# Kernel optimization log

Hardware: AMD Instinct MI355X
Metric: run time of the kernel (lower is better)

The kernel has to match this reference:

```python
import jax, jax.numpy as jnp
import numpy as np
import math

N, T, D, H = 2, 4096, 768, 12
DH = D // H


def setup_inputs() -> dict:
    key = jax.random.key(0)
    ks = jax.random.split(key, 6)
    x = jax.random.normal(ks[0], (N, T, D), dtype=jnp.float32)
    # key-padding mask: True = masked out; mask the last quarter of positions
    mask = jnp.broadcast_to(jnp.arange(T) >= (3 * T) // 4, (N, T))
    scale = 0.02
    Wq = jax.random.normal(ks[1], (D, D), dtype=jnp.float32) * scale
    Wk = jax.random.normal(ks[2], (D, D), dtype=jnp.float32) * scale
    Wv = jax.random.normal(ks[3], (D, D), dtype=jnp.float32) * scale
    Wo = jax.random.normal(ks[4], (D, D), dtype=jnp.float32) * scale
    zb = jnp.zeros((D,), dtype=jnp.float32)
    return {"x": x, "mask": mask, "Wq": Wq, "bq": zb, "Wk": Wk, "bk": zb,
            "Wv": Wv, "bv": zb, "Wo": Wo, "bo": zb}


def reference(x, mask, Wq, bq, Wk, bk, Wv, bv, Wo, bo):
    n, t, d = x.shape
    h, dh = H, d // H
    # torch Linear: y = x @ W.T + b
    def proj(W, b):
        return (x @ W.T + b).reshape(n, t, h, dh).transpose(0, 2, 1, 3)  # [n,h,t,dh]
    q = proj(Wq, bq)
    k = proj(Wk, bk)
    v = proj(Wv, bv)
    s = jnp.einsum('nhqd,nhkd->nhqk', q, k) / math.sqrt(dh)  # [n,h,t,t]
    s = jnp.where(mask[:, None, None, :], -jnp.inf, s)
    p = jax.nn.softmax(s, axis=-1)
    # dropout prob 0.0 / eval mode -> identity
    a = jnp.einsum('nhqk,nhkd->nhqd', p, v)  # [n,h,t,dh]
    a = a.transpose(0, 2, 1, 3).reshape(n, t, d)
    return a @ Wo.T + bo
```

## Files before the change

kernel.cpp:

```cpp
#include <hip/hip_runtime.h>
#include <hip/hip_bf16.h>
#include <stdint.h>

#define T_SEQ 4096
#define DM    768
#define NHEAD 12
#define DHEAD 64
#define NBAT  2
#define LOG2E 1.4426950408889634f

typedef __bf16 bf16x8 __attribute__((ext_vector_type(8)));
typedef float  f32x4  __attribute__((ext_vector_type(4)));

static __device__ __forceinline__ unsigned short f2bf(float f) {
  unsigned int u = __builtin_bit_cast(unsigned int, f);
  u += 0x7FFFu + ((u >> 16) & 1u);
  return (unsigned short)(u >> 16);
}
static __device__ __forceinline__ unsigned short f2bf_hw(float f) {
  __hip_bfloat16 h = __float2bfloat16(f);
  return __builtin_bit_cast(unsigned short, h);
}
static __device__ __forceinline__ unsigned int pk2(float lo, float hi) {
  return (unsigned int)f2bf_hw(lo) | ((unsigned int)f2bf_hw(hi) << 16);
}
static __device__ __forceinline__ void gll16(const void* g, void* l) {
  __builtin_amdgcn_global_load_lds(
      (const __attribute__((address_space(1))) unsigned int*)g,
      (__attribute__((address_space(3))) unsigned int*)l, 16, 0, 0);
}
static __device__ __forceinline__ bf16x8 ldfrag(const unsigned short* p) {
  const unsigned short* q = (const unsigned short*)__builtin_assume_aligned(p, 16);
  bf16x8 v;
  __builtin_memcpy(&v, q, 16);
  return v;
}
static __device__ __forceinline__ void st8(unsigned short* p, uint2 v) {
  __builtin_memcpy(__builtin_assume_aligned(p, 8), &v, 8);
}
static __device__ __forceinline__ uint2 ld8(const unsigned short* p) {
  uint2 v;
  __builtin_memcpy(&v, __builtin_assume_aligned(p, 8), 8);
  return v;
}

__global__ void cvt_kernel(const float* __restrict__ s, unsigned short* __restrict__ d, int n) {
  int i = (blockIdx.x * 256 + threadIdx.x) * 4;
  if (i < n) {
    float4 v = *(const float4*)(s + i);
    ushort4 o;
    o.x = f2bf(v.x); o.y = f2bf(v.y); o.z = f2bf(v.z); o.w = f2bf(v.w);
    *(ushort4*)(d + i) = o;
  }
}
__global__ void cvt4_kernel(const float* __restrict__ s0, const float* __restrict__ s1,
                            const float* __restrict__ s2, const float* __restrict__ s3,
                            unsigned short* __restrict__ d0, unsigned short* __restrict__ d1,
                            unsigned short* __restrict__ d2, unsigned short* __restrict__ d3,
                            int n) {
  int w = blockIdx.y;
  const float* sp = (w == 0) ? s0 : (w == 1) ? s1 : (w == 2) ? s2 : s3;
  unsigned short* dp = (w == 0) ? d0 : (w == 1) ? d1 : (w == 2) ? d2 : d3;
  int i = (blockIdx.x * 256 + threadIdx.x) * 4;
  if (i < n) {
    float4 v = *(const float4*)(sp + i);
    ushort4 o;
    o.x = f2bf(v.x); o.y = f2bf(v.y); o.z = f2bf(v.z); o.w = f2bf(v.w);
    *(ushort4*)(dp + i) = o;
  }
}

__global__ void init_kernel(int* __restrict__ kmx) {
  if (threadIdx.x < NBAT) { kmx[threadIdx.x] = 0; kmx[NBAT + threadIdx.x] = T_SEQ; }
}

__global__ void build_bias_kernel(const unsigned char* __restrict__ mraw,
                                  float* __restrict__ bias,
                                  int* __restrict__ kmx) {
  int idx = blockIdx.x * 256 + threadIdx.x;
  int is_u8 = (mraw[(3 * T_SEQ) / 4] != 0);
  int masked;
  if (is_u8) masked = (mraw[idx] != 0);
  else       masked = (((const int*)mraw)[idx] != 0);
  bias[idx] = masked ? -1e9f : 0.0f;
  __shared__ int smax, smin;
  if (threadIdx.x == 0) { smax = 0; smin = T_SEQ; }
  __syncthreads();
  int pos = idx & (T_SEQ - 1);
  if (!masked) atomicMax(&smax, pos + 1);
  else         atomicMin(&smin, pos);
  __syncthreads();
  if (threadIdx.x == 0) {
    atomicMax(&kmx[idx >> 12], smax);
    atomicMin(&kmx[NBAT + (idx >> 12)], smin);
  }
}

template <int MODE>
__global__ __launch_bounds__(256, 2) void gemm128(
    const unsigned short* __restrict__ A,
    const unsigned short* __restrict__ W0, const unsigned short* __restrict__ W1,
    const unsigned short* __restrict__ W2,
    const float* __restrict__ Bb0, const float* __restrict__ Bb1,
    const float* __restrict__ Bb2,
    void* __restrict__ O0, void* __restrict__ O1, void* __restrict__ O2) {
  constexpr int NT = (MODE == 0) ? 8 : 4;
  constexpr int NROWS = NT * 32;
  __shared__ __align__(16) unsigned short lA[128 * 64];
  __shared__ __align__(16) unsigned short lB[NROWS * 64];
  const int t = threadIdx.x;
  const int lane = t & 63, quad = lane >> 4, l16 = lane & 15;
  const int wave = t >> 6;
  const int moff = (wave & 1) * 64, noff = (wave >> 1) * (NT * 16);
  const int m0 = blockIdx.x * 128;
  const int by = blockIdx.y;
  const unsigned short* W;
  const float* Bb;
  int o0, wsel = 0;
  if constexpr (MODE == 0) {
    wsel = by / 3;
    o0 = (by % 3) * 256;
    W  = (wsel == 0) ? W0  : ((wsel == 1) ? W1  : W2);
    Bb = (wsel == 0) ? Bb0 : ((wsel == 1) ? Bb1 : Bb2);
  } else {
    o0 = by * 128; W = W0; Bb = Bb0;
  }
  f32x4 acc[4][NT];
#pragma unroll
  for (int i = 0; i < 4; ++i)
#pragma unroll
    for (int j = 0; j < NT; ++j) acc[i][j] = (f32x4){0.f, 0.f, 0.f, 0.f};

  for (int k0 = 0; k0 < DM; k0 += 64) {
#pragma unroll
    for (int i = 0; i < 4; ++i) {
      int c = i * 256 + t;
      int r = c >> 3;
      int qc = (c & 7) ^ (r & 7);
      gll16(A + (size_t)(m0 + r) * DM + k0 + qc * 8, &lA[(i * 256 + (t & 192)) * 8]);
    }
#pragma unroll
    for (int i = 0; i < NT; ++i) {
      int c = i * 256 + t;
      int r = c >> 3;
      int qc = (c & 7) ^ (r & 7);
      gll16(W + (size_t)(o0 + r) * DM + k0 + qc * 8, &lB[(i * 256 + (t & 192)) * 8]);
    }
    __syncthreads();
    bf16x8 af[4][2];
#pragma unroll
    for (int mt = 0; mt < 4; ++mt) {
      int r = moff + mt * 16 + l16;
#pragma unroll
      for (int s = 0; s < 2; ++s)
        af[mt][s] = ldfrag(&lA[(r * 8 + ((s * 4 + quad) ^ (r & 7))) * 8]);
    }
#pragma unroll
    for (int nt = 0; nt < NT; ++nt) {
      int r = noff + nt * 16 + l16;
      bf16x8 b0 = ldfrag(&lB[(r * 8 + ((quad) ^ (r & 7))) * 8]);
      bf16x8 b1 = ldfrag(&lB[(r * 8 + ((4 + quad) ^ (r & 7))) * 8]);
#pragma unroll
      for (int mt = 0; mt < 4; ++mt) {
        acc[mt][nt] = __builtin_amdgcn_mfma_f32_16x16x32_bf16(af[mt][0], b0, acc[mt][nt], 0, 0, 0);
        acc[mt][nt] = __builtin_amdgcn_mfma_f32_16x16x32_bf16(af[mt][1], b1, acc[mt][nt], 0, 0, 0);
      }
    }
    __syncthreads();
  }
#pragma unroll
  for (int nt = 0; nt < NT; ++nt) {
    int o = o0 + noff + nt * 16 + l16;
    float bias = Bb[o];
    if (MODE == 0 && wsel == 2) {
      int h = o >> 6, d = o & 63;
#pragma unroll
      for (int mt = 0; mt < 4; ++mt) {
        int m = m0 + moff + mt * 16 + quad * 4;
        int n = m >> 12, tb = m & (T_SEQ - 1);
        uint2 w;
        w.x = pk2(acc[mt][nt][0] + bias, acc[mt][nt][1] + bias);
        w.y = pk2(acc[mt][nt][2] + bias, acc[mt][nt][3] + bias);
        *(uint2*)((unsigned short*)O2 +
                  ((size_t)(n * NHEAD + h) * DHEAD + d) * T_SEQ + tb) = w;
      }
      continue;
    }
#pragma unroll
    for (int mt = 0; mt < 4; ++mt) {
#pragma unroll
      for (int r = 0; r < 4; ++r) {
        int m = m0 + moff + mt * 16 + quad * 4 + r;
        float v = acc[mt][nt][r] + bias;
        if constexpr (MODE == 0) {
          int n = m >> 12, tt = m & (T_SEQ - 1);
          int h = o >> 6, d = o & 63;
          if (wsel == 0)
            ((unsigned short*)O0)[((size_t)(n * NHEAD + h) * T_SEQ + tt) * DHEAD + d] = f2bf(v * (0.125f * LOG2E));
          else
            ((unsigned short*)O1)[((size_t)(n * NHEAD + h) * T_SEQ + tt) * DHEAD + d] = f2bf(v);
        } else {
          ((float*)O0)[(size_t)m * DM + o] = v;
        }
      }
    }
  }
}

__global__ __launch_bounds__(256, 3) void flash_kernel(
    const unsigned short* __restrict__ Q, const unsigned short* __restrict__ K,
    const unsigned short* __restrict__ VT, const float* __restrict__ bias,
    const int* __restrict__ kmx, unsigned short* __restrict__ Aout) {
  __shared__ __align__(16) unsigned short lK[128 * 64];
  __shared__ __align__(16) unsigned short lV[64 * 128];
  const int t = threadIdx.x;
  const int lane = t & 63, quad = lane >> 4, l16 = lane & 15;
  const int wave = t >> 6;
  const int nh = blockIdx.y;
  const int n = nh / NHEAD, h = nh % NHEAD;
  const int q0 = blockIdx.x * 128;
  const size_t base = (size_t)nh * T_SEQ * DHEAD;

  bf16x8 qf[2][2];
#pragma unroll
  for (int qt = 0; qt < 2; ++qt) {
    int qrow = q0 + wave * 32 + qt * 16 + l16;
    qf[qt][0] = ldfrag(Q + base + (size_t)qrow * DHEAD + quad * 8);
    qf[qt][1] = ldfrag(Q + base + (size_t)qrow * DHEAD + 32 + quad * 8);
  }

  bf16x8 vone;
#pragma unroll
  for (int i = 0; i < 8; ++i) vone[i] = (__bf16)1.0f;

  f32x4 oacc[2][4], oaccl[2];
#pragma unroll
  for (int qt = 0; qt < 2; ++qt) {
#pragma unroll
    for (int dt = 0; dt < 4; ++dt) oacc[qt][dt] = (f32x4){0.f, 0.f, 0.f, 0.f};
    oaccl[qt] = (f32x4){0.f, 0.f, 0.f, 0.f};
  }

  const int km = kmx[n], fm = kmx[NBAT + n];
  int ntiles = (km + 127) >> 7;
  if (ntiles > (T_SEQ >> 7)) ntiles = T_SEQ >> 7;
  const float* brow = bias + (size_t)n * T_SEQ;

  const int idxA = ((((quad & 1) << 1) * 16) + l16) << 2;
  const int idxB = idxA + 64;
  const bool hiq = (quad >= 2);

  for (int it = 0; it < ntiles; ++it) {
    const int j0 = it << 7;
#pragma unroll
    for (int i = 0; i < 4; ++i) {
      int c = i * 256 + t;
      int r = c >> 3;
      int qc = (c & 7) ^ (r & 7);
      gll16(K + base + (size_t)(j0 + r) * DHEAD + qc * 8, &lK[(i * 256 + (t & 192)) * 8]);
    }
#pragma unroll
    for (int i = 0; i < 4; ++i) {
      int c = i * 256 + t;
      int r = c >> 4;
      int qc = (c & 15) ^ (r & 15);
      gll16(VT + base + (size_t)r * T_SEQ + j0 + qc * 8, &lV[(i * 256 + (t & 192)) * 8]);
    }
    __syncthreads();

    f32x4 sacc[2][8];
#pragma unroll
    for (int qt = 0; qt < 2; ++qt)
#pragma unroll
      for (int nt = 0; nt < 8; ++nt) sacc[qt][nt] = (f32x4){0.f, 0.f, 0.f, 0.f};
#pragma unroll
    for (int nt = 0; nt < 8; ++nt) {
      int r = nt * 16 + l16;
      bf16x8 k0f = ldfrag(&lK[(r * 8 + (quad ^ (r & 7))) * 8]);
      bf16x8 k1f = ldfrag(&lK[(r * 8 + ((4 + quad) ^ (r & 7))) * 8]);
#pragma unroll
      for (int qt = 0; qt < 2; ++qt) {
        sacc[qt][nt] = __builtin_amdgcn_mfma_f32_16x16x32_bf16(k0f, qf[qt][0], sacc[qt][nt], 0, 0, 0);
        sacc[qt][nt] = __builtin_amdgcn_mfma_f32_16x16x32_bf16(k1f, qf[qt][1], sacc[qt][nt], 0, 0, 0);
      }
    }
    if (j0 + 128 > fm) {
#pragma unroll
      for (int nt = 0; nt < 8; ++nt) {
        float4 bv = *(const float4*)&brow[j0 + nt * 16 + quad * 4];
#pragma unroll
        for (int qt = 0; qt < 2; ++qt) {
          sacc[qt][nt][0] += bv.x; sacc[qt][nt][1] += bv.y;
          sacc[qt][nt][2] += bv.z; sacc[qt][nt][3] += bv.w;
        }
      }
    }
    unsigned int pd[2][8][2];
#pragma unroll
    for (int qt = 0; qt < 2; ++qt)
#pragma unroll
      for (int nt = 0; nt < 8; ++nt) {
        pd[qt][nt][0] = pk2(__builtin_exp2f(sacc[qt][nt][0]), __builtin_exp2f(sacc[qt][nt][1]));
        pd[qt][nt][1] = pk2(__builtin_exp2f(sacc[qt][nt][2]), __builtin_exp2f(sacc[qt][nt][3]));
      }
#pragma unroll
    for (int kb = 0; kb < 4; ++kb) {
      bf16x8 pb[2];
#pragma unroll
      for (int qt = 0; qt < 2; ++qt) {
        unsigned int t0, t1;
        uint4 bw;
        t0 = (unsigned int)__builtin_amdgcn_ds_bpermute(idxA, (int)pd[qt][2 * kb][0]);
        t1 = (unsigned int)__builtin_amdgcn_ds_bpermute(idxA, (int)pd[qt][2 * kb + 1][0]);
        bw.x = hiq ? t1 : t0;
        t0 = (unsigned int)__builtin_amdgcn_ds_bpermute(idxA, (int)pd[qt][2 * kb][1]);
        t1 = (unsigned int)__builtin_amdgcn_ds_bpermute(idxA, (int)pd[qt][2 * kb + 1][1]);
        bw.y = hiq ? t1 : t0;
        t0 = (unsigned int)__builtin_amdgcn_ds_bpermute(idxB, (int)pd[qt][2 * kb][0]);
        t1 = (unsigned int)__builtin_amdgcn_ds_bpermute(idxB, (int)pd[qt][2 * kb + 1][0]);
        bw.z = hiq ? t1 : t0;
        t0 = (unsigned int)__builtin_amdgcn_ds_bpermute(idxB, (int)pd[qt][2 * kb][1]);
        t1 = (unsigned int)__builtin_amdgcn_ds_bpermute(idxB, (int)pd[qt][2 * kb + 1][1]);
        bw.w = hiq ? t1 : t0;
        pb[qt] = __builtin_bit_cast(bf16x8, bw);
      }
#pragma unroll
      for (int dt = 0; dt < 4; ++dt) {
        int rv = dt * 16 + l16;
        bf16x8 vf = ldfrag(&lV[(rv * 16 + ((kb * 4 + quad) ^ (rv & 15))) * 8]);
#pragma unroll
        for (int qt = 0; qt < 2; ++qt)
          oacc[qt][dt] = __builtin_amdgcn_mfma_f32_16x16x32_bf16(vf, pb[qt], oacc[qt][dt], 0, 0, 0);
      }
#pragma unroll
      for (int qt = 0; qt < 2; ++qt)
        oaccl[qt] = __builtin_amdgcn_mfma_f32_16x16x32_bf16(vone, pb[qt], oaccl[qt], 0, 0, 0);
    }
    __syncthreads();
  }
  unsigned short* lO = &lK[wave * (32 * 68)];
#pragma unroll
  for (int qt = 0; qt < 2; ++qt) {
    float l = oaccl[qt][0];
    float rl = (l > 0.f) ? 1.0f / l : 0.f;
#pragma unroll
    for (int dt = 0; dt < 4; ++dt) {
      uint2 w;
      w.x = pk2(oacc[qt][dt][0] * rl, oacc[qt][dt][1] * rl);
      w.y = pk2(oacc[qt][dt][2] * rl, oacc[qt][dt][3] * rl);
      st8(lO + (qt * 16 + l16) * 68 + dt * 16 + quad * 4, w);
    }
  }
#pragma unroll
  for (int it2 = 0; it2 < 8; ++it2) {
    int rowq = it2 * 4 + quad;
    uint2 w = ld8(lO + rowq * 68 + l16 * 4);
    int tt = q0 + wave * 32 + rowq;
    *(uint2*)(Aout + (size_t)(n * T_SEQ + tt) * DM + h * DHEAD + l16 * 4) = w;
  }
}

extern "C" void kernel_launch(void* const* d_in, const int* in_sizes, int n_in,
                              void* d_out, int out_size, void* d_ws, size_t ws_size,
                              hipStream_t stream) {
  const float*         x  = (const float*)d_in[0];
  const unsigned char* mk = (const unsigned char*)d_in[1];
  const float* Wq = (const float*)d_in[2];
  const float* bq = (const float*)d_in[3];
  const float* Wk = (const float*)d_in[4];
  const float* bk = (const float*)d_in[5];
  const float* Wv = (const float*)d_in[6];
  const float* bv = (const float*)d_in[7];
  const float* Wo = (const float*)d_in[8];
  const float* bo = (const float*)d_in[9];

  const int xe = NBAT * T_SEQ * DM;
  const int we = DM * DM;
  const size_t xb_bytes = (size_t)xe * 2;
  const size_t wb_bytes = (size_t)we * 2;
  const size_t kv_bytes = (size_t)NBAT * NHEAD * T_SEQ * DHEAD * 2;

  auto rnd = [](size_t b) { return (b + 255) & ~(size_t)255; };
  size_t need = rnd(xb_bytes) + 4 * rnd(wb_bytes) + 2 * rnd(kv_bytes) +
                rnd((size_t)NBAT * T_SEQ * 4) + 256;
  if (ws_size < need) return;

  char* ws = (char*)d_ws;
  size_t off = 0;
  auto alloc = [&](size_t b) { char* p = ws + off; off += rnd(b); return p; };
  unsigned short* x_b  = (unsigned short*)alloc(xb_bytes);
  unsigned short* wq_b = (unsigned short*)alloc(wb_bytes);
  unsigned short* wk_b = (unsigned short*)alloc(wb_bytes);
  unsigned short* wv_b = (unsigned short*)alloc(wb_bytes);
  unsigned short* wo_b = (unsigned short*)alloc(wb_bytes);
  unsigned short* k_ws  = (unsigned short*)alloc(kv_bytes);
  unsigned short* vt_ws = (unsigned short*)alloc(kv_bytes);
  float* bias = (float*)alloc((size_t)NBAT * T_SEQ * 4);
  int* kmx    = (int*)alloc(256);
  unsigned short* q_ws = (unsigned short*)d_out;
  unsigned short* a_ws = x_b;

  init_kernel<<<1, 64, 0, stream>>>(kmx);
  cvt_kernel<<<xe / 1024, 256, 0, stream>>>(x, x_b, xe);
  cvt4_kernel<<<dim3(we / 1024, 4), 256, 0, stream>>>(
      Wq, Wk, Wv, Wo, wq_b, wk_b, wv_b, wo_b, we);
  build_bias_kernel<<<(NBAT * T_SEQ) / 256, 256, 0, stream>>>(mk, bias, kmx);
  gemm128<0><<<dim3((NBAT * T_SEQ) / 128, 9), 256, 0, stream>>>(
      x_b, wq_b, wk_b, wv_b, bq, bk, bv, q_ws, k_ws, vt_ws);
  flash_kernel<<<dim3(T_SEQ / 128, NBAT * NHEAD), 256, 0, stream>>>(
      q_ws, k_ws, vt_ws, bias, kmx, a_ws);
  gemm128<1><<<dim3((NBAT * T_SEQ) / 128, DM / 128), 256, 0, stream>>>(
      a_ws, wo_b, wo_b, wo_b, bo, bo, bo, d_out, d_out, d_out);
  (void)in_sizes; (void)n_in; (void)out_size;
}
```

Before: 316.1 us.

## Use single-wave flash blocks reading K/V directly and retile projection GEMMs

The flash kernel becomes one wave per block covering 32 query rows. It drops the LDS staging of K and V and the block barriers, loading MFMA fragments straight from global memory. Block indices are remapped so that neighbouring blocks share heads, which is meant to help L2 reuse of K/V. Separately, both GEMMs get narrower N tiles (192 and 96 columns) with more blocks in the grid, and the QKV GEMM's occupancy bound is raised to 3. The risk is that many more uncoalesced global loads of K/V replace shared-memory reuse across four waves.

```diff
diff --git a/kernel.cpp b/kernel.cpp
--- a/kernel.cpp
+++ b/kernel.cpp
@@ -97,14 +97,14 @@
 }
 
 template <int MODE>
-__global__ __launch_bounds__(256, 2) void gemm128(
+__global__ __launch_bounds__(256, (MODE == 0) ? 3 : 2) void gemm128(
     const unsigned short* __restrict__ A,
     const unsigned short* __restrict__ W0, const unsigned short* __restrict__ W1,
     const unsigned short* __restrict__ W2,
     const float* __restrict__ Bb0, const float* __restrict__ Bb1,
     const float* __restrict__ Bb2,
     void* __restrict__ O0, void* __restrict__ O1, void* __restrict__ O2) {
-  constexpr int NT = (MODE == 0) ? 8 : 4;
+  constexpr int NT = (MODE == 0) ? 6 : 3;
   constexpr int NROWS = NT * 32;
   __shared__ __align__(16) unsigned short lA[128 * 64];
   __shared__ __align__(16) unsigned short lB[NROWS * 64];
@@ -118,12 +118,12 @@
   const float* Bb;
   int o0, wsel = 0;
   if constexpr (MODE == 0) {
-    wsel = by / 3;
-    o0 = (by % 3) * 256;
+    wsel = by >> 2;
+    o0 = (by & 3) * 192;
     W  = (wsel == 0) ? W0  : ((wsel == 1) ? W1  : W2);
     Bb = (wsel == 0) ? Bb0 : ((wsel == 1) ? Bb1 : Bb2);
   } else {
-    o0 = by * 128; W = W0; Bb = Bb0;
+    o0 = by * 96; W = W0; Bb = Bb0;
   }
   f32x4 acc[4][NT];
 #pragma unroll
@@ -207,24 +207,26 @@
   }
 }
 
-__global__ __launch_bounds__(256, 3) void flash_kernel(
+__global__ __launch_bounds__(64, 3) void flash_kernel(
     const unsigned short* __restrict__ Q, const unsigned short* __restrict__ K,
     const unsigned short* __restrict__ VT, const float* __restrict__ bias,
     const int* __restrict__ kmx, unsigned short* __restrict__ Aout) {
-  __shared__ __align__(16) unsigned short lK[128 * 64];
-  __shared__ __align__(16) unsigned short lV[64 * 128];
-  const int t = threadIdx.x;
-  const int lane = t & 63, quad = lane >> 4, l16 = lane & 15;
-  const int wave = t >> 6;
-  const int nh = blockIdx.y;
-  const int n = nh / NHEAD, h = nh % NHEAD;
-  const int q0 = blockIdx.x * 128;
+  __shared__ __align__(16) unsigned short lO[32 * 68];
+  const int lane = threadIdx.x;
+  const int quad = lane >> 4, l16 = lane & 15;
+  const int b = blockIdx.x;
+  const int slot = b >> 3;
+  const int nh = (b & 7) * 3 + (slot % 3);
+  const int q0 = (slot / 3) * 32;
+  const int n = nh / NHEAD, h = nh - n * NHEAD;
   const size_t base = (size_t)nh * T_SEQ * DHEAD;
+  const unsigned short* Kb = K + base + (size_t)l16 * DHEAD + quad * 8;
+  const unsigned short* Vb = VT + base + (size_t)l16 * T_SEQ + quad * 8;
 
   bf16x8 qf[2][2];
 #pragma unroll
   for (int qt = 0; qt < 2; ++qt) {
-    int qrow = q0 + wave * 32 + qt * 16 + l16;
+    int qrow = q0 + qt * 16 + l16;
     qf[qt][0] = ldfrag(Q + base + (size_t)qrow * DHEAD + quad * 8);
     qf[qt][1] = ldfrag(Q + base + (size_t)qrow * DHEAD + 32 + quad * 8);
   }
@@ -252,22 +254,6 @@
 
   for (int it = 0; it < ntiles; ++it) {
     const int j0 = it << 7;
-#pragma unroll
-    for (int i = 0; i < 4; ++i) {
-      int c = i * 256 + t;
-      int r = c >> 3;
-      int qc = (c & 7) ^ (r & 7);
-      gll16(K + base + (size_t)(j0 + r) * DHEAD + qc * 8, &lK[(i * 256 + (t & 192)) * 8]);
-    }
-#pragma unroll
-    for (int i = 0; i < 4; ++i) {
-      int c = i * 256 + t;
-      int r = c >> 4;
-      int qc = (c & 15) ^ (r & 15);
-      gll16(VT + base + (size_t)r * T_SEQ + j0 + qc * 8, &lV[(i * 256 + (t & 192)) * 8]);
-    }
-    __syncthreads();
-
     f32x4 sacc[2][8];
 #pragma unroll
     for (int qt = 0; qt < 2; ++qt)
@@ -275,9 +261,9 @@
       for (int nt = 0; nt < 8; ++nt) sacc[qt][nt] = (f32x4){0.f, 0.f, 0.f, 0.f};
 #pragma unroll
     for (int nt = 0; nt < 8; ++nt) {
-      int r = nt * 16 + l16;
-      bf16x8 k0f = ldfrag(&lK[(r * 8 + (quad ^ (r & 7))) * 8]);
-      bf16x8 k1f = ldfrag(&lK[(r * 8 + ((4 + quad) ^ (r & 7))) * 8]);
+      const unsigned short* kr = Kb + (size_t)(j0 + nt * 16) * DHEAD;
+      bf16x8 k0f = ldfrag(kr);
+      bf16x8 k1f = ldfrag(kr + 32);
 #pragma unroll
       for (int qt = 0; qt < 2; ++qt) {
         sacc[qt][nt] = __builtin_amdgcn_mfma_f32_16x16x32_bf16(k0f, qf[qt][0], sacc[qt][nt], 0, 0, 0);
@@ -326,8 +312,7 @@
       }
 #pragma unroll
       for (int dt = 0; dt < 4; ++dt) {
-        int rv = dt * 16 + l16;
-        bf16x8 vf = ldfrag(&lV[(rv * 16 + ((kb * 4 + quad) ^ (rv & 15))) * 8]);
+        bf16x8 vf = ldfrag(Vb + (size_t)(dt * 16) * T_SEQ + j0 + kb * 32);
 #pragma unroll
         for (int qt = 0; qt < 2; ++qt)
           oacc[qt][dt] = __builtin_amdgcn_mfma_f32_16x16x32_bf16(vf, pb[qt], oacc[qt][dt], 0, 0, 0);
@@ -336,9 +321,7 @@
       for (int qt = 0; qt < 2; ++qt)
         oaccl[qt] = __builtin_amdgcn_mfma_f32_16x16x32_bf16(vone, pb[qt], oaccl[qt], 0, 0, 0);
     }
-    __syncthreads();
-  }
-  unsigned short* lO = &lK[wave * (32 * 68)];
+  }
 #pragma unroll
   for (int qt = 0; qt < 2; ++qt) {
     float l = oaccl[qt][0];
@@ -355,7 +338,7 @@
   for (int it2 = 0; it2 < 8; ++it2) {
     int rowq = it2 * 4 + quad;
     uint2 w = ld8(lO + rowq * 68 + l16 * 4);
-    int tt = q0 + wave * 32 + rowq;
+    int tt = q0 + rowq;
     *(uint2*)(Aout + (size_t)(n * T_SEQ + tt) * DM + h * DHEAD + l16 * 4) = w;
   }
 }
@@ -405,11 +388,11 @@
   cvt4_kernel<<<dim3(we / 1024, 4), 256, 0, stream>>>(
       Wq, Wk, Wv, Wo, wq_b, wk_b, wv_b, wo_b, we);
   build_bias_kernel<<<(NBAT * T_SEQ) / 256, 256, 0, stream>>>(mk, bias, kmx);
-  gemm128<0><<<dim3((NBAT * T_SEQ) / 128, 9), 256, 0, stream>>>(
+  gemm128<0><<<dim3((NBAT * T_SEQ) / 128, 12), 256, 0, stream>>>(
       x_b, wq_b, wk_b, wv_b, bq, bk, bv, q_ws, k_ws, vt_ws);
-  flash_kernel<<<dim3(T_SEQ / 128, NBAT * NHEAD), 256, 0, stream>>>(
+  flash_kernel<<<dim3(NBAT * NHEAD * (T_SEQ / 32) / 3 * 3 / 8 * 8 == 0 ? 3072 : 3072), 64, 0, stream>>>(
       q_ws, k_ws, vt_ws, bias, kmx, a_ws);
-  gemm128<1><<<dim3((NBAT * T_SEQ) / 128, DM / 128), 256, 0, stream>>>(
+  gemm128<1><<<dim3((NBAT * T_SEQ) / 128, 8), 256, 0, stream>>>(
       a_ws, wo_b, wo_b, wo_b, bo, bo, bo, d_out, d_out, d_out);
   (void)in_sizes; (void)n_in; (void)out_size;
 }
```

After: 410.0 us. +29.7%, slower.
